# Kernel tuning notes

Measured on AMD Instinct MI355X. Metric: run time of the kernel, lower is better.

Reference implementation:

```python
import jax, jax.numpy as jnp
import numpy as np


def setup_inputs() -> dict:
    key = jax.random.key(0)
    k1, k2, k3, k4 = jax.random.split(key, 4)
    B, T, C, H = 8, 2048, 1024, 64
    x = jax.random.normal(k1, (B, T, C), dtype=jnp.float32)
    Wq = jax.random.normal(k2, (C, H), dtype=jnp.float32) * (C ** -0.5)
    Wk = jax.random.normal(k3, (C, H), dtype=jnp.float32) * (C ** -0.5)
    Wv = jax.random.normal(k4, (C, H), dtype=jnp.float32) * (C ** -0.5)
    return {"x": x, "Wq": Wq, "Wk": Wk, "Wv": Wv}


def reference(x, Wq, Wk, Wv):
    # x: [B,T,C]; Wq/Wk/Wv: [C,H] (nn.Linear bias=False => x @ W)
    B, T, C = x.shape
    H = Wq.shape[-1]
    q = jnp.einsum('btc,ch->bth', x, Wq)
    k = jnp.einsum('btc,ch->bth', x, Wk)
    v = jnp.einsum('btc,ch->bth', x, Wv)
    scale = H ** -0.5
    att = jnp.einsum('bqh,bkh->bqk', q, k) * scale  # [B,T,T]
    causal = jnp.tril(jnp.ones((T, T), dtype=bool))
    att = jnp.where(causal, att, -jnp.inf)
    att = jax.nn.softmax(att, axis=-1)
    out = jnp.einsum('bqk,bkh->bqh', att, v)  # [B,T,H]
    return out
```

## Files before the change

kernel.cpp:

```cpp
#include <hip/hip_runtime.h>
#include <hip/hip_bf16.h>
#include <math.h>

#define BB 8
#define TT 2048
#define CC 1024
#define HH 64
#define BT (BB * TT)

typedef __attribute__((ext_vector_type(8))) short short8;
typedef __attribute__((ext_vector_type(4))) float floatx4;

static __device__ inline ushort f2bf(float f) {
    __hip_bfloat16 h = __float2bfloat16(f);
    return *reinterpret_cast<ushort*>(&h);
}
static __device__ inline unsigned int f2bf2(float lo, float hi) {
    __hip_bfloat162 h = __float22bfloat162_rn(make_float2(lo, hi));
    return *reinterpret_cast<unsigned int*>(&h);
}
static __device__ inline float bf2f(ushort u) {
    union { unsigned int i; float f; } c;
    c.i = ((unsigned int)u) << 16;
    return c.f;
}

__global__ __launch_bounds__(256) void wprep_kernel(
    const float* __restrict__ Wq, const float* __restrict__ Wk,
    const float* __restrict__ Wv, ushort* __restrict__ WbT)
{
    __shared__ float ws_[64 * 65];
    const int m  = blockIdx.x >> 4;
    const int kb = (blockIdx.x & 15) * 64;
    const float* W = (m == 0) ? Wq : (m == 1) ? Wk : Wv;
    const int t  = threadIdx.x;
    const int lr = t >> 4, lc = (t & 15) * 4;
    #pragma unroll
    for (int i = 0; i < 4; ++i) {
        const int row = lr + i * 16;
        float4 v = *(const float4*)&W[(size_t)(kb + row) * HH + lc];
        ws_[row * 65 + lc + 0] = v.x; ws_[row * 65 + lc + 1] = v.y;
        ws_[row * 65 + lc + 2] = v.z; ws_[row * 65 + lc + 3] = v.w;
    }
    __syncthreads();
    const int n = t & 63, kseg = t >> 6;
    union { ushort s[16]; uint4 q[2]; } u;
    #pragma unroll
    for (int j = 0; j < 16; ++j)
        u.s[j] = f2bf(ws_[(kseg * 16 + j) * 65 + n]);
    ushort* dst = &WbT[(size_t)(m * 64 + n) * 1024 + kb + kseg * 16];
    *(uint4*)&dst[0] = u.q[0];
    *(uint4*)&dst[8] = u.q[1];
}

__global__ __launch_bounds__(256) void qkv_kernel(
    const float* __restrict__ x, const ushort* __restrict__ WbT,
    ushort* __restrict__ qb, ushort* __restrict__ kbS, ushort* __restrict__ vS)
{
    __shared__ ushort As[2][256 * 8];

    const int row0 = blockIdx.x * 32;
    const int t    = threadIdx.x;
    const int w    = t >> 6;
    const int lane = t & 63;
    const int l16  = lane & 15;
    const int quad = lane >> 4;
    const int ct0  = w * 3;

    const int srow = t >> 3, sseg = t & 7;
    const int slot = (((sseg >> 2) * 2 + (srow >> 4)) * 16 + (srow & 15)) * 4 + (sseg & 3);
    const float* xsrc = &x[(size_t)(row0 + srow) * CC + sseg * 8];

    floatx4 acc[2][3];
    #pragma unroll
    for (int mt = 0; mt < 2; ++mt)
        #pragma unroll
        for (int c = 0; c < 3; ++c) acc[mt][c] = (floatx4){0.f, 0.f, 0.f, 0.f};

    float4 xa0 = *(const float4*)&xsrc[0];
    float4 xb0 = *(const float4*)&xsrc[4];
    float4 xa1 = *(const float4*)&xsrc[64];
    float4 xb1 = *(const float4*)&xsrc[68];

    short8 bfr[2][3];
    #pragma unroll
    for (int p = 0; p < 2; ++p)
        #pragma unroll
        for (int c = 0; c < 3; ++c)
            bfr[p][c] = *(const short8*)&WbT[(size_t)((ct0 + c) * 16 + l16) * 1024
                                             + p * 32 + quad * 8];

    auto body = [&](int it, float4& xa, float4& xb) {
        uint4 uq;
        uq.x = f2bf2(xa.x, xa.y); uq.y = f2bf2(xa.z, xa.w);
        uq.z = f2bf2(xb.x, xb.y); uq.w = f2bf2(xb.z, xb.w);
        *(uint4*)&As[it & 1][slot * 8] = uq;
        __syncthreads();

        if (it + 2 < 16) {
            xa = *(const float4*)&xsrc[(it + 2) * 64 + 0];
            xb = *(const float4*)&xsrc[(it + 2) * 64 + 4];
        }
        short8 bnx[2][3];
        if (it < 15) {
            const int kn = (it + 1) * 64;
            #pragma unroll
            for (int p = 0; p < 2; ++p)
                #pragma unroll
                for (int c = 0; c < 3; ++c)
                    bnx[p][c] = *(const short8*)&WbT[(size_t)((ct0 + c) * 16 + l16) * 1024
                                                     + kn + p * 32 + quad * 8];
        }

        #pragma unroll
        for (int p = 0; p < 2; ++p) {
            short8 a0 = *(const short8*)&As[it & 1][(size_t)((p * 2 + 0) * 64 + l16 * 4 + quad) * 8];
            short8 a1 = *(const short8*)&As[it & 1][(size_t)((p * 2 + 1) * 64 + l16 * 4 + quad) * 8];
            #pragma unroll
            for (int c = 0; c < 3; ++c) {
                acc[0][c] = __builtin_amdgcn_mfma_f32_16x16x32_bf16(a0, bfr[p][c], acc[0][c], 0, 0, 0);
                acc[1][c] = __builtin_amdgcn_mfma_f32_16x16x32_bf16(a1, bfr[p][c], acc[1][c], 0, 0, 0);
            }
        }
        #pragma unroll
        for (int p = 0; p < 2; ++p)
            #pragma unroll
            for (int c = 0; c < 3; ++c)
                bfr[p][c] = bnx[p][c];
    };

    for (int it2 = 0; it2 < 16; it2 += 2) {
        body(it2 + 0, xa0, xb0);
        body(it2 + 1, xa1, xb1);
    }

    const int half = (row0 >> 5) & 1;
    const size_t tile = (size_t)(row0 >> 6) * 4096;
    #pragma unroll
    for (int c = 0; c < 3; ++c) {
        const int ct    = ct0 + c;
        const int mtype = ct >> 2;
        const int n0    = (ct & 3) * 16;
        #pragma unroll
        for (int mt = 0; mt < 2; ++mt) {
            const int row = row0 + mt * 16 + quad * 4;
            if (mtype == 0) {
                #pragma unroll
                for (int reg = 0; reg < 4; ++reg)
                    qb[(size_t)(row + reg) * HH + n0 + l16] = f2bf(acc[mt][c][reg] * 0.125f);
            } else if (mtype == 1) {
                const int cP    = half * 2 + mt;
                const int pP    = (ct & 3) >> 1;
                const int quadP = ((ct & 3) * 2 + (l16 >> 3)) & 3;
                const int jP    = l16 & 7;
                const int ub    = (cP * 2 + pP) * 64 + quadP * 16;
                #pragma unroll
                for (int reg = 0; reg < 4; ++reg)
                    kbS[tile + (size_t)(ub + quad * 4 + reg) * 8 + jP] = f2bf(acc[mt][c][reg]);
            } else {
                const int cp2 = (ct & 3) * 2 + half;
                #pragma unroll
                for (int reg = 0; reg < 4; ++reg) {
                    const int rq    = quad * 4 + reg;
                    const int quadP = mt * 2 + (rq >> 3);
                    vS[tile + (size_t)(cp2 * 64 + quadP * 16 + l16) * 8 + (rq & 7)] = f2bf(acc[mt][c][reg]);
                }
            }
        }
    }
}

__global__ __launch_bounds__(256) void attn_kernel(
    const ushort* __restrict__ qb, const ushort* __restrict__ kbS,
    const ushort* __restrict__ vS, ushort* __restrict__ Opart,
    float* __restrict__ ml)
{
    __shared__ __align__(16) ushort P[4][16 * 72];

    const int t    = threadIdx.x;
    const int w    = t >> 6;
    const int lane = t & 63;
    const int l16  = lane & 15;
    const int quad = lane >> 4;

    const int b   = blockIdx.x & 7;
    const int idx = blockIdx.x >> 3;
    int qt, part, np;
    if (idx < 32)      { qt = 31 - (idx >> 2); part = idx & 3; np = 4; }
    else if (idx < 56) { const int u = idx - 32; const int g = u / 3;
                         qt = 23 - g; part = u - g * 3; np = 3; }
    else if (idx < 72) { const int u = idx - 56; qt = 15 - (u >> 1); part = u & 1; np = 2; }
    else               { qt = 7 - (idx - 72); part = 0; np = 1; }
    const int ntiles = qt + 1;
    const int ktb = (part * ntiles) / np;
    const int kte = ((part + 1) * ntiles) / np;

    const ushort* ktile0 = kbS + (size_t)(b * 32) * 4096;
    const ushort* vtile0 = vS  + (size_t)(b * 32) * 4096;

    short8 qf[2];
    {
        const ushort* qrow = qb + ((size_t)b * TT + qt * 64 + w * 16) * HH;
        qf[0] = *(const short8*)&qrow[l16 * HH + quad * 8];
        qf[1] = *(const short8*)&qrow[l16 * HH + 32 + quad * 8];
    }
    short8 ones;
    #pragma unroll
    for (int i = 0; i < 8; ++i) ones[i] = (short)0x3F80;

    floatx4 o[4], osum;
    #pragma unroll
    for (int c = 0; c < 4; ++c) o[c] = (floatx4){0.f, 0.f, 0.f, 0.f};
    osum = (floatx4){0.f, 0.f, 0.f, 0.f};

    ushort* Pw = &P[w][0];

    for (int kt = ktb; kt < kte; ++kt) {
        const ushort* kg = ktile0 + (size_t)kt * 4096;
        const ushort* vg = vtile0 + (size_t)kt * 4096;

        short8 kf[4][2], vf[4][2];
        #pragma unroll
        for (int c = 0; c < 4; ++c)
            #pragma unroll
            for (int p = 0; p < 2; ++p) {
                kf[c][p] = *(const short8*)&kg[(size_t)(((c * 2 + p) * 64) + lane) * 8];
                vf[c][p] = *(const short8*)&vg[(size_t)(((c * 2 + p) * 64) + lane) * 8];
            }

        floatx4 s[4];
        #pragma unroll
        for (int c = 0; c < 4; ++c) s[c] = (floatx4){0.f, 0.f, 0.f, 0.f};
        __builtin_amdgcn_s_setprio(1);
        #pragma unroll
        for (int c = 0; c < 4; ++c)
            #pragma unroll
            for (int p = 0; p < 2; ++p)
                s[c] = __builtin_amdgcn_mfma_f32_16x16x32_bf16(kf[c][p], qf[p], s[c], 0, 0, 0);
        __builtin_amdgcn_s_setprio(0);

        if (kt == ntiles - 1) {
            const int key0 = kt * 64 + quad * 4;
            const int qrow = qt * 64 + w * 16 + l16;
            #pragma unroll
            for (int c = 0; c < 4; ++c)
                #pragma unroll
                for (int reg = 0; reg < 4; ++reg)
                    if (key0 + c * 16 + reg > qrow) s[c][reg] = -1e30f;
        }

        #pragma unroll
        for (int c = 0; c < 4; ++c) {
            uint2 u;
            u.x = f2bf2(__expf(s[c][0]), __expf(s[c][1]));
            u.y = f2bf2(__expf(s[c][2]), __expf(s[c][3]));
            *(uint2*)&Pw[l16 * 72 + c * 16 + quad * 4] = u;
        }

        short8 pf[2];
        pf[0] = *(const short8*)&Pw[l16 * 72 + quad * 8];
        pf[1] = *(const short8*)&Pw[l16 * 72 + 32 + quad * 8];

        __builtin_amdgcn_s_setprio(1);
        #pragma unroll
        for (int p = 0; p < 2; ++p) {
            #pragma unroll
            for (int c = 0; c < 4; ++c)
                o[c] = __builtin_amdgcn_mfma_f32_16x16x32_bf16(pf[p], vf[c][p], o[c], 0, 0, 0);
            osum = __builtin_amdgcn_mfma_f32_16x16x32_bf16(pf[p], ones, osum, 0, 0, 0);
        }
        __builtin_amdgcn_s_setprio(0);
    }

    const size_t ub = (size_t)blockIdx.x * 4096;
    #pragma unroll
    for (int c = 0; c < 4; ++c)
        #pragma unroll
        for (int reg = 0; reg < 4; ++reg)
            Opart[ub + (w * 16 + quad * 4 + reg) * 64 + c * 16 + l16] = f2bf(o[c][reg]);
    if (l16 == 0) {
        #pragma unroll
        for (int reg = 0; reg < 4; ++reg)
            ml[(size_t)blockIdx.x * 64 + w * 16 + quad * 4 + reg] = osum[reg];
    }
}

__global__ __launch_bounds__(256) void merge_kernel(
    const ushort* __restrict__ Opart, const float* __restrict__ ml,
    float* __restrict__ out)
{
    const int t    = threadIdx.x;
    const int gw   = blockIdx.x * 4 + (t >> 6);
    const int lane = t & 63;
    const int b    = gw >> 8;
    const int v    = gw & 255;
    const int qt   = v >> 3;
    const int oct  = v & 7;

    int base, np;
    if (qt >= 24)      { base = (31 - qt) * 4;      np = 4; }
    else if (qt >= 16) { base = 32 + (23 - qt) * 3; np = 3; }
    else if (qt >= 8)  { base = 56 + (15 - qt) * 2; np = 2; }
    else               { base = 72 + (7 - qt);      np = 1; }

    const int r4 = lane >> 4;
    const int cs = (lane & 15) * 4;
    float* obase = out + ((size_t)b * TT + qt * 64) * HH;

    #pragma unroll
    for (int rg = 0; rg < 2; ++rg) {
        const int row = oct * 8 + rg * 4 + r4;
        float den = 0.f;
        float ax = 0.f, ay = 0.f, az = 0.f, aw = 0.f;
        for (int p = 0; p < np; ++p) {
            const int unit = (base + p) * 8 + b;
            den += ml[(size_t)unit * 64 + row];
            ushort4 ov = *(const ushort4*)&Opart[(size_t)unit * 4096 + row * 64 + cs];
            ax += bf2f(ov.x); ay += bf2f(ov.y); az += bf2f(ov.z); aw += bf2f(ov.w);
        }
        const float inv = 1.0f / den;
        float4 o4;
        o4.x = ax * inv; o4.y = ay * inv; o4.z = az * inv; o4.w = aw * inv;
        *(float4*)&obase[(size_t)row * HH + cs] = o4;
    }
}

extern "C" void kernel_launch(void* const* d_in, const int* in_sizes, int n_in,
                              void* d_out, int out_size, void* d_ws, size_t ws_size,
                              hipStream_t stream)
{
    (void)in_sizes; (void)n_in; (void)out_size; (void)ws_size;
    const float* x  = (const float*)d_in[0];
    const float* Wq = (const float*)d_in[1];
    const float* Wk = (const float*)d_in[2];
    const float* Wv = (const float*)d_in[3];
    float* outp = (float*)d_out;

    char* base = (char*)d_ws;
    ushort* WbT   = (ushort*)(base);
    ushort* qbuf  = (ushort*)(base + 393216);
    ushort* kbS   = qbuf + (size_t)BT * HH;
    ushort* vSb   = kbS + (size_t)BT * HH;
    ushort* Opart = vSb + (size_t)BT * HH;
    float*  ml    = (float*)((char*)Opart + (size_t)640 * 4096 * 2);

    wprep_kernel<<<dim3(48),  256, 0, stream>>>(Wq, Wk, Wv, WbT);
    qkv_kernel  <<<dim3(512), 256, 0, stream>>>(x, WbT, qbuf, kbS, vSb);
    attn_kernel <<<dim3(640), 256, 0, stream>>>(qbuf, kbS, vSb, Opart, ml);
    merge_kernel<<<dim3(512), 256, 0, stream>>>(Opart, ml, outp);
}
```

Before: 140.0 us.

## Load QKV A-fragments directly from global, defer V loads, transpose partial output layout

The QKV projection kernel no longer stages bf16-converted x through double-buffered shared memory with a barrier each step. Each lane now loads its MFMA A-fragment straight from global memory, converts it in registers, and prefetches the next k-step. In attention, V fragments are loaded after the QK MFMAs, which lowers peak register pressure. The partial-output store is transposed to packed 8-byte writes, and the merge kernel reads it in that transposed layout, loading the row sums as float4. Costs are less coalesced global reads of x in the projection and strided scalar stores in merge.

```diff
diff --git a/kernel.cpp b/kernel.cpp
--- a/kernel.cpp
+++ b/kernel.cpp
@@ -57,8 +57,6 @@
     const float* __restrict__ x, const ushort* __restrict__ WbT,
     ushort* __restrict__ qb, ushort* __restrict__ kbS, ushort* __restrict__ vS)
 {
-    __shared__ ushort As[2][256 * 8];
-
     const int row0 = blockIdx.x * 32;
     const int t    = threadIdx.x;
     const int w    = t >> 6;
@@ -67,22 +65,26 @@
     const int quad = lane >> 4;
     const int ct0  = w * 3;
 
-    const int srow = t >> 3, sseg = t & 7;
-    const int slot = (((sseg >> 2) * 2 + (srow >> 4)) * 16 + (srow & 15)) * 4 + (sseg & 3);
-    const float* xsrc = &x[(size_t)(row0 + srow) * CC + sseg * 8];
-
     floatx4 acc[2][3];
     #pragma unroll
     for (int mt = 0; mt < 2; ++mt)
         #pragma unroll
         for (int c = 0; c < 3; ++c) acc[mt][c] = (floatx4){0.f, 0.f, 0.f, 0.f};
 
-    float4 xa0 = *(const float4*)&xsrc[0];
-    float4 xb0 = *(const float4*)&xsrc[4];
-    float4 xa1 = *(const float4*)&xsrc[64];
-    float4 xb1 = *(const float4*)&xsrc[68];
-
-    short8 bfr[2][3];
+    const float* xr0 = &x[(size_t)(row0 + l16) * CC + quad * 8];
+    const float* xr1 = xr0 + 16 * CC;
+
+    float4 xc[4][2], xn[4][2];
+    #pragma unroll
+    for (int mt = 0; mt < 2; ++mt)
+        #pragma unroll
+        for (int p = 0; p < 2; ++p) {
+            const float* src = (mt ? xr1 : xr0) + p * 32;
+            xc[mt * 2 + p][0] = *(const float4*)&src[0];
+            xc[mt * 2 + p][1] = *(const float4*)&src[4];
+        }
+
+    short8 bfr[2][3], bnx[2][3];
     #pragma unroll
     for (int p = 0; p < 2; ++p)
         #pragma unroll
@@ -90,20 +92,17 @@
             bfr[p][c] = *(const short8*)&WbT[(size_t)((ct0 + c) * 16 + l16) * 1024
                                              + p * 32 + quad * 8];
 
-    auto body = [&](int it, float4& xa, float4& xb) {
-        uint4 uq;
-        uq.x = f2bf2(xa.x, xa.y); uq.y = f2bf2(xa.z, xa.w);
-        uq.z = f2bf2(xb.x, xb.y); uq.w = f2bf2(xb.z, xb.w);
-        *(uint4*)&As[it & 1][slot * 8] = uq;
-        __syncthreads();
-
-        if (it + 2 < 16) {
-            xa = *(const float4*)&xsrc[(it + 2) * 64 + 0];
-            xb = *(const float4*)&xsrc[(it + 2) * 64 + 4];
-        }
-        short8 bnx[2][3];
+    for (int it = 0; it < 16; ++it) {
         if (it < 15) {
             const int kn = (it + 1) * 64;
+            #pragma unroll
+            for (int mt = 0; mt < 2; ++mt)
+                #pragma unroll
+                for (int p = 0; p < 2; ++p) {
+                    const float* src = (mt ? xr1 : xr0) + kn + p * 32;
+                    xn[mt * 2 + p][0] = *(const float4*)&src[0];
+                    xn[mt * 2 + p][1] = *(const float4*)&src[4];
+                }
             #pragma unroll
             for (int p = 0; p < 2; ++p)
                 #pragma unroll
@@ -112,26 +111,35 @@
                                                      + kn + p * 32 + quad * 8];
         }
 
-        #pragma unroll
-        for (int p = 0; p < 2; ++p) {
-            short8 a0 = *(const short8*)&As[it & 1][(size_t)((p * 2 + 0) * 64 + l16 * 4 + quad) * 8];
-            short8 a1 = *(const short8*)&As[it & 1][(size_t)((p * 2 + 1) * 64 + l16 * 4 + quad) * 8];
+        short8 afr[2][2];
+        #pragma unroll
+        for (int mt = 0; mt < 2; ++mt)
+            #pragma unroll
+            for (int p = 0; p < 2; ++p) {
+                const float4 a = xc[mt * 2 + p][0];
+                const float4 b = xc[mt * 2 + p][1];
+                union { unsigned int u[4]; short8 s; } cv;
+                cv.u[0] = f2bf2(a.x, a.y); cv.u[1] = f2bf2(a.z, a.w);
+                cv.u[2] = f2bf2(b.x, b.y); cv.u[3] = f2bf2(b.z, b.w);
+                afr[mt][p] = cv.s;
+            }
+
+        __builtin_amdgcn_s_setprio(1);
+        #pragma unroll
+        for (int p = 0; p < 2; ++p)
             #pragma unroll
             for (int c = 0; c < 3; ++c) {
-                acc[0][c] = __builtin_amdgcn_mfma_f32_16x16x32_bf16(a0, bfr[p][c], acc[0][c], 0, 0, 0);
-                acc[1][c] = __builtin_amdgcn_mfma_f32_16x16x32_bf16(a1, bfr[p][c], acc[1][c], 0, 0, 0);
+                acc[0][c] = __builtin_amdgcn_mfma_f32_16x16x32_bf16(afr[0][p], bfr[p][c], acc[0][c], 0, 0, 0);
+                acc[1][c] = __builtin_amdgcn_mfma_f32_16x16x32_bf16(afr[1][p], bfr[p][c], acc[1][c], 0, 0, 0);
             }
-        }
+        __builtin_amdgcn_s_setprio(0);
+
+        #pragma unroll
+        for (int i = 0; i < 4; ++i) { xc[i][0] = xn[i][0]; xc[i][1] = xn[i][1]; }
         #pragma unroll
         for (int p = 0; p < 2; ++p)
             #pragma unroll
-            for (int c = 0; c < 3; ++c)
-                bfr[p][c] = bnx[p][c];
-    };
-
-    for (int it2 = 0; it2 < 16; it2 += 2) {
-        body(it2 + 0, xa0, xb0);
-        body(it2 + 1, xa1, xb1);
+            for (int c = 0; c < 3; ++c) bfr[p][c] = bnx[p][c];
     }
 
     const int half = (row0 >> 5) & 1;
@@ -219,14 +227,12 @@
         const ushort* kg = ktile0 + (size_t)kt * 4096;
         const ushort* vg = vtile0 + (size_t)kt * 4096;
 
-        short8 kf[4][2], vf[4][2];
+        short8 kf[4][2];
         #pragma unroll
         for (int c = 0; c < 4; ++c)
             #pragma unroll
-            for (int p = 0; p < 2; ++p) {
+            for (int p = 0; p < 2; ++p)
                 kf[c][p] = *(const short8*)&kg[(size_t)(((c * 2 + p) * 64) + lane) * 8];
-                vf[c][p] = *(const short8*)&vg[(size_t)(((c * 2 + p) * 64) + lane) * 8];
-            }
 
         floatx4 s[4];
         #pragma unroll
@@ -238,6 +244,13 @@
             for (int p = 0; p < 2; ++p)
                 s[c] = __builtin_amdgcn_mfma_f32_16x16x32_bf16(kf[c][p], qf[p], s[c], 0, 0, 0);
         __builtin_amdgcn_s_setprio(0);
+
+        short8 vf[4][2];
+        #pragma unroll
+        for (int c = 0; c < 4; ++c)
+            #pragma unroll
+            for (int p = 0; p < 2; ++p)
+                vf[c][p] = *(const short8*)&vg[(size_t)(((c * 2 + p) * 64) + lane) * 8];
 
         if (kt == ntiles - 1) {
             const int key0 = kt * 64 + quad * 4;
@@ -273,15 +286,18 @@
     }
 
     const size_t ub = (size_t)blockIdx.x * 4096;
-    #pragma unroll
-    for (int c = 0; c < 4; ++c)
+    const int rbase = w * 16 + quad * 4;
+    #pragma unroll
+    for (int c = 0; c < 4; ++c) {
+        uint2 u;
+        u.x = f2bf2(o[c][0], o[c][1]);
+        u.y = f2bf2(o[c][2], o[c][3]);
+        *(uint2*)&Opart[ub + (size_t)(c * 16 + l16) * 64 + rbase] = u;
+    }
+    if (l16 == 0) {
         #pragma unroll
         for (int reg = 0; reg < 4; ++reg)
-            Opart[ub + (w * 16 + quad * 4 + reg) * 64 + c * 16 + l16] = f2bf(o[c][reg]);
-    if (l16 == 0) {
-        #pragma unroll
-        for (int reg = 0; reg < 4; ++reg)
-            ml[(size_t)blockIdx.x * 64 + w * 16 + quad * 4 + reg] = osum[reg];
+            ml[(size_t)blockIdx.x * 64 + rbase + reg] = osum[reg];
     }
 }
 
@@ -303,25 +319,24 @@
     else if (qt >= 8)  { base = 56 + (15 - qt) * 2; np = 2; }
     else               { base = 72 + (7 - qt);      np = 1; }
 
-    const int r4 = lane >> 4;
-    const int cs = (lane & 15) * 4;
     float* obase = out + ((size_t)b * TT + qt * 64) * HH;
 
     #pragma unroll
     for (int rg = 0; rg < 2; ++rg) {
-        const int row = oct * 8 + rg * 4 + r4;
-        float den = 0.f;
+        const int row0 = oct * 8 + rg * 4;
+        float dx = 0.f, dy = 0.f, dz = 0.f, dw = 0.f;
         float ax = 0.f, ay = 0.f, az = 0.f, aw = 0.f;
         for (int p = 0; p < np; ++p) {
             const int unit = (base + p) * 8 + b;
-            den += ml[(size_t)unit * 64 + row];
-            ushort4 ov = *(const ushort4*)&Opart[(size_t)unit * 4096 + row * 64 + cs];
+            float4 d = *(const float4*)&ml[(size_t)unit * 64 + row0];
+            dx += d.x; dy += d.y; dz += d.z; dw += d.w;
+            ushort4 ov = *(const ushort4*)&Opart[(size_t)unit * 4096 + lane * 64 + row0];
             ax += bf2f(ov.x); ay += bf2f(ov.y); az += bf2f(ov.z); aw += bf2f(ov.w);
         }
-        const float inv = 1.0f / den;
-        float4 o4;
-        o4.x = ax * inv; o4.y = ay * inv; o4.z = az * inv; o4.w = aw * inv;
-        *(float4*)&obase[(size_t)row * HH + cs] = o4;
+        obase[(size_t)(row0 + 0) * HH + lane] = ax / dx;
+        obase[(size_t)(row0 + 1) * HH + lane] = ay / dy;
+        obase[(size_t)(row0 + 2) * HH + lane] = az / dz;
+        obase[(size_t)(row0 + 3) * HH + lane] = aw / dw;
     }
 }
 
```

Result: slower. 158.6 us (+13.2%).

## Transpose partial-output layout, defer V loads, lighten QKV barrier and reorder MFMAs

Applied to the files above, without the earlier changes.

Partial attention outputs are now stored transposed, with each lane writing packed bf16 pairs instead of scattered scalar stores. The merge kernel reads them to match, loads the denominators as float4 and writes one column per lane. In the attention loop, V fragments are now loaded after the QK MFMAs, which shortens their register lifetime and may cut register pressure. The QKV kernel swaps __syncthreads for an explicit lgkmcnt wait plus s_barrier, loads all A fragments up front and runs its MFMAs at raised priority. The merge output stores are now strided per lane, which may lower write coalescing.

```diff
diff --git a/kernel.cpp b/kernel.cpp
--- a/kernel.cpp
+++ b/kernel.cpp
@@ -23,6 +23,10 @@
     union { unsigned int i; float f; } c;
     c.i = ((unsigned int)u) << 16;
     return c.f;
+}
+static __device__ inline void lds_barrier() {
+    asm volatile("s_waitcnt lgkmcnt(0)" ::: "memory");
+    __builtin_amdgcn_s_barrier();
 }
 
 __global__ __launch_bounds__(256) void wprep_kernel(
@@ -57,7 +61,7 @@
     const float* __restrict__ x, const ushort* __restrict__ WbT,
     ushort* __restrict__ qb, ushort* __restrict__ kbS, ushort* __restrict__ vS)
 {
-    __shared__ ushort As[2][256 * 8];
+    __shared__ __align__(16) ushort As[2][256 * 8];
 
     const int row0 = blockIdx.x * 32;
     const int t    = threadIdx.x;
@@ -95,7 +99,7 @@
         uq.x = f2bf2(xa.x, xa.y); uq.y = f2bf2(xa.z, xa.w);
         uq.z = f2bf2(xb.x, xb.y); uq.w = f2bf2(xb.z, xb.w);
         *(uint4*)&As[it & 1][slot * 8] = uq;
-        __syncthreads();
+        lds_barrier();
 
         if (it + 2 < 16) {
             xa = *(const float4*)&xsrc[(it + 2) * 64 + 0];
@@ -112,16 +116,21 @@
                                                      + kn + p * 32 + quad * 8];
         }
 
-        #pragma unroll
-        for (int p = 0; p < 2; ++p) {
-            short8 a0 = *(const short8*)&As[it & 1][(size_t)((p * 2 + 0) * 64 + l16 * 4 + quad) * 8];
-            short8 a1 = *(const short8*)&As[it & 1][(size_t)((p * 2 + 1) * 64 + l16 * 4 + quad) * 8];
-            #pragma unroll
-            for (int c = 0; c < 3; ++c) {
-                acc[0][c] = __builtin_amdgcn_mfma_f32_16x16x32_bf16(a0, bfr[p][c], acc[0][c], 0, 0, 0);
-                acc[1][c] = __builtin_amdgcn_mfma_f32_16x16x32_bf16(a1, bfr[p][c], acc[1][c], 0, 0, 0);
-            }
-        }
+        short8 a0 = *(const short8*)&As[it & 1][(size_t)((0 * 2 + 0) * 64 + l16 * 4 + quad) * 8 + 0];
+        short8 a1 = *(const short8*)&As[it & 1][(size_t)((0 * 2 + 1) * 64 + l16 * 4 + quad) * 8 + 0];
+        short8 a2 = *(const short8*)&As[it & 1][(size_t)((1 * 2 + 0) * 64 + l16 * 4 + quad) * 8 + 0];
+        short8 a3 = *(const short8*)&As[it & 1][(size_t)((1 * 2 + 1) * 64 + l16 * 4 + quad) * 8 + 0];
+
+        __builtin_amdgcn_s_setprio(1);
+        #pragma unroll
+        for (int c = 0; c < 3; ++c) {
+            acc[0][c] = __builtin_amdgcn_mfma_f32_16x16x32_bf16(a0, bfr[0][c], acc[0][c], 0, 0, 0);
+            acc[1][c] = __builtin_amdgcn_mfma_f32_16x16x32_bf16(a1, bfr[0][c], acc[1][c], 0, 0, 0);
+            acc[0][c] = __builtin_amdgcn_mfma_f32_16x16x32_bf16(a2, bfr[1][c], acc[0][c], 0, 0, 0);
+            acc[1][c] = __builtin_amdgcn_mfma_f32_16x16x32_bf16(a3, bfr[1][c], acc[1][c], 0, 0, 0);
+        }
+        __builtin_amdgcn_s_setprio(0);
+
         #pragma unroll
         for (int p = 0; p < 2; ++p)
             #pragma unroll
@@ -219,14 +228,12 @@
         const ushort* kg = ktile0 + (size_t)kt * 4096;
         const ushort* vg = vtile0 + (size_t)kt * 4096;
 
-        short8 kf[4][2], vf[4][2];
+        short8 kf[4][2];
         #pragma unroll
         for (int c = 0; c < 4; ++c)
             #pragma unroll
-            for (int p = 0; p < 2; ++p) {
+            for (int p = 0; p < 2; ++p)
                 kf[c][p] = *(const short8*)&kg[(size_t)(((c * 2 + p) * 64) + lane) * 8];
-                vf[c][p] = *(const short8*)&vg[(size_t)(((c * 2 + p) * 64) + lane) * 8];
-            }
 
         floatx4 s[4];
         #pragma unroll
@@ -238,6 +245,13 @@
             for (int p = 0; p < 2; ++p)
                 s[c] = __builtin_amdgcn_mfma_f32_16x16x32_bf16(kf[c][p], qf[p], s[c], 0, 0, 0);
         __builtin_amdgcn_s_setprio(0);
+
+        short8 vf[4][2];
+        #pragma unroll
+        for (int c = 0; c < 4; ++c)
+            #pragma unroll
+            for (int p = 0; p < 2; ++p)
+                vf[c][p] = *(const short8*)&vg[(size_t)(((c * 2 + p) * 64) + lane) * 8];
 
         if (kt == ntiles - 1) {
             const int key0 = kt * 64 + quad * 4;
@@ -273,15 +287,18 @@
     }
 
     const size_t ub = (size_t)blockIdx.x * 4096;
-    #pragma unroll
-    for (int c = 0; c < 4; ++c)
+    const int rbase = w * 16 + quad * 4;
+    #pragma unroll
+    for (int c = 0; c < 4; ++c) {
+        uint2 u;
+        u.x = f2bf2(o[c][0], o[c][1]);
+        u.y = f2bf2(o[c][2], o[c][3]);
+        *(uint2*)&Opart[ub + (size_t)(c * 16 + l16) * 64 + rbase] = u;
+    }
+    if (l16 == 0) {
         #pragma unroll
         for (int reg = 0; reg < 4; ++reg)
-            Opart[ub + (w * 16 + quad * 4 + reg) * 64 + c * 16 + l16] = f2bf(o[c][reg]);
-    if (l16 == 0) {
-        #pragma unroll
-        for (int reg = 0; reg < 4; ++reg)
-            ml[(size_t)blockIdx.x * 64 + w * 16 + quad * 4 + reg] = osum[reg];
+            ml[(size_t)blockIdx.x * 64 + rbase + reg] = osum[reg];
     }
 }
 
@@ -303,25 +320,24 @@
     else if (qt >= 8)  { base = 56 + (15 - qt) * 2; np = 2; }
     else               { base = 72 + (7 - qt);      np = 1; }
 
-    const int r4 = lane >> 4;
-    const int cs = (lane & 15) * 4;
     float* obase = out + ((size_t)b * TT + qt * 64) * HH;
 
     #pragma unroll
     for (int rg = 0; rg < 2; ++rg) {
-        const int row = oct * 8 + rg * 4 + r4;
-        float den = 0.f;
+        const int row0 = oct * 8 + rg * 4;
+        float dx = 0.f, dy = 0.f, dz = 0.f, dw = 0.f;
         float ax = 0.f, ay = 0.f, az = 0.f, aw = 0.f;
         for (int p = 0; p < np; ++p) {
             const int unit = (base + p) * 8 + b;
-            den += ml[(size_t)unit * 64 + row];
-            ushort4 ov = *(const ushort4*)&Opart[(size_t)unit * 4096 + row * 64 + cs];
+            float4 d = *(const float4*)&ml[(size_t)unit * 64 + row0];
+            dx += d.x; dy += d.y; dz += d.z; dw += d.w;
+            ushort4 ov = *(const ushort4*)&Opart[(size_t)unit * 4096 + lane * 64 + row0];
             ax += bf2f(ov.x); ay += bf2f(ov.y); az += bf2f(ov.z); aw += bf2f(ov.w);
         }
-        const float inv = 1.0f / den;
-        float4 o4;
-        o4.x = ax * inv; o4.y = ay * inv; o4.z = az * inv; o4.w = aw * inv;
-        *(float4*)&obase[(size_t)row * HH + cs] = o4;
+        obase[(size_t)(row0 + 0) * HH + lane] = ax / dx;
+        obase[(size_t)(row0 + 1) * HH + lane] = ay / dy;
+        obase[(size_t)(row0 + 2) * HH + lane] = az / dz;
+        obase[(size_t)(row0 + 3) * HH + lane] = aw / dw;
     }
 }
 
```

Result: no change. 138.2 us (-1.3%).
